# Optimization experiments

Measured on AMD Instinct MI355X. Metric: run time of the kernel, lower is better.

## Reference

```python
import jax, jax.numpy as jnp
import numpy as np

CAPACITY_FACTOR = 1.25
TOP_K = 2


def setup_inputs() -> dict:
    key = jax.random.key(0)
    ks = jax.random.split(key, 4)
    B, T, D, H, N = 8, 8192, 512, 512, 32
    x = jax.random.normal(ks[0], (B, T, D), jnp.float32)
    Wg = jax.random.normal(ks[1], (D, N), jnp.float32) * 0.02   # gate (no bias)
    W1 = jax.random.normal(ks[2], (N, D, H), jnp.float32) * 0.02  # stacked expert fc1
    b1 = jnp.zeros((N, H), jnp.float32)
    W2 = jax.random.normal(ks[3], (N, H, D), jnp.float32) * 0.02  # stacked expert fc2
    b2 = jnp.zeros((N, D), jnp.float32)
    return {"x": x, "Wg": Wg, "W1": W1, "b1": b1, "W2": W2, "b2": b2}


def _moe(x, Wg, W1, b1, W2, b2):
    B, T, D = x.shape
    N = Wg.shape[1]
    K = TOP_K
    BT = B * T
    BTK = BT * K
    C = int(np.ceil(CAPACITY_FACTOR * BTK / N))  # capacity per expert (static)

    x_flat = x.reshape(BT, D)
    probs = jax.nn.softmax(x_flat @ Wg, axis=-1)            # [BT, N]
    vals, idx = jax.lax.top_k(probs, K)                     # [BT, K]
    vals = vals / jnp.clip(vals.sum(-1, keepdims=True), 1e-9)  # normalize_gates

    # Assignments in the exact order of the original double loop: pos-major, j-minor.
    a = idx.reshape(BTK)                                    # expert id per assignment
    oh = jax.nn.one_hot(a, N, dtype=jnp.int32)              # [BTK, N]
    rank = jnp.cumsum(oh, axis=0) - oh                      # prior count for each expert
    pos = jnp.take_along_axis(rank, a[:, None], axis=1)[:, 0]  # slot within expert
    keep = pos < C                                          # capacity-limited dispatch
    dest = jnp.where(keep, a * C + pos, N * C)              # OOB sentinel -> dropped
    token = jnp.arange(BTK) // K                            # source token per assignment

    # Dispatch: scatter kept tokens into per-expert capacity buffers [N, C, D].
    buf = jnp.zeros((N * C, D), x.dtype).at[dest].set(x_flat[token], mode="drop")
    buf = buf.reshape(N, C, D)

    # Expert FFN (grouped GEMMs). FeedForwardExpert assumed Linear-ReLU-Linear.
    h = jax.nn.relu(jnp.einsum("ncd,ndh->nch", buf, W1) + b1[:, None, :])
    o = (jnp.einsum("nch,nhd->ncd", h, W2) + b2[:, None, :]).reshape(N * C, D)

    # Combine: gather expert outputs, weight by gates, scatter-add back by token.
    gathered = o[jnp.minimum(dest, N * C - 1)]              # dropped rows zeroed via w
    w = vals.reshape(BTK) * keep.astype(x.dtype)
    y_flat = jax.ops.segment_sum(gathered * w[:, None], token, num_segments=BT)
    contrib = jax.ops.segment_sum(w, token, num_segments=BT)
    # Tokens with no surviving assignment pass through unchanged.
    y_flat = jnp.where(contrib[:, None] <= 1e-12, x_flat, y_flat)
    return y_flat.reshape(B, T, D)


def reference(x, Wg, W1, b1, W2, b2):
    return _moe(x, Wg, W1, b1, W2, b2)
```

## Files before the change

kernel.cpp:

```cpp
#include <hip/hip_runtime.h>
#include <hip/hip_bf16.h>

#define BT 65536
#define DD 512
#define HH 512
#define NE 32
#define CAP 5120
#define BM 64
#define NRB 80

typedef float  f32x4  __attribute__((ext_vector_type(4)));
typedef short  bf16x8 __attribute__((ext_vector_type(8)));

__device__ __forceinline__ unsigned short f2bf(float f){
    unsigned int u = __builtin_bit_cast(unsigned int, f);
    unsigned int r = (u + 0x7fffu + ((u >> 16) & 1u)) >> 16;
    return (unsigned short)r;
}
__device__ __forceinline__ float bf2f(unsigned short h){
    unsigned int u = ((unsigned int)h) << 16;
    return __builtin_bit_cast(float, u);
}

__global__ __launch_bounds__(256) void k_prep(
    const float* __restrict__ x, const float* __restrict__ Wg,
    const float* __restrict__ W1, const float* __restrict__ W2,
    unsigned short* __restrict__ W1f, unsigned short* __restrict__ W2f,
    int* __restrict__ counts, int* __restrict__ gsl, float* __restrict__ wts,
    unsigned char* __restrict__ flags, unsigned short* __restrict__ xb16)
{
    __shared__ float pacc[4][64][36];
    __shared__ int lcnt[NE], lbase[NE];

    int tid = threadIdx.x;

    if (blockIdx.x < 512){
        int b = blockIdx.x;
        int w = b >> 8;
        int e = (b >> 3) & 31;
        int kq = b & 7;
        const float* src = (w ? W2 : W1) + ((size_t)e << 18);
        unsigned short* dst = (w ? W2f : W1f) + ((size_t)e << 18);
        #pragma unroll 1
        for (int kg = 0; kg < 8; kg++){
            int k0 = kq*64 + kg*8;
            #pragma unroll
            for (int ng = 0; ng < 2; ng++){
                int n = ng*256 + tid;
                unsigned short v[8];
                #pragma unroll
                for (int j = 0; j < 8; j++)
                    v[j] = f2bf(src[(size_t)(k0 + j)*512 + n]);
                int nt = n >> 4, kc = k0 >> 5, ln = ((k0 >> 3) & 3)*16 + (n & 15);
                *(bf16x8*)(dst + (((size_t)(nt*16 + kc)*64 + ln) << 3)) = *(bf16x8*)v;
            }
        }
        return;
    }

    int blk = blockIdx.x - 512;
    int l   = tid & 63;
    int q   = __builtin_amdgcn_readfirstlane(tid >> 6);
    int tok = blk*64 + l;

    const float* xq = x + (size_t)tok*DD + q*128;

    float acc[NE];
    #pragma unroll
    for (int n = 0; n < NE; n++) acc[n] = 0.f;

    float4 xa = *(const float4*)(xq);
    float4 xb = *(const float4*)(xq + 4);
    #pragma unroll 1
    for (int d = 0; d < 128; d += 8){
        int dn = (d + 8 < 128) ? (d + 8) : 0;
        float4 na = *(const float4*)(xq + dn);
        float4 nb = *(const float4*)(xq + dn + 4);
        uint4 pk;
        pk.x = (unsigned)f2bf(xa.x) | ((unsigned)f2bf(xa.y) << 16);
        pk.y = (unsigned)f2bf(xa.z) | ((unsigned)f2bf(xa.w) << 16);
        pk.z = (unsigned)f2bf(xb.x) | ((unsigned)f2bf(xb.y) << 16);
        pk.w = (unsigned)f2bf(xb.z) | ((unsigned)f2bf(xb.w) << 16);
        *(uint4*)(xb16 + (size_t)tok*DD + q*128 + d) = pk;
        #pragma unroll
        for (int j = 0; j < 8; j++){
            float xv = (j < 4) ? ((j==0)?xa.x:(j==1)?xa.y:(j==2)?xa.z:xa.w)
                               : ((j==4)?xb.x:(j==5)?xb.y:(j==6)?xb.z:xb.w);
            const float4* wr = (const float4*)(Wg + (size_t)(q*128 + d + j)*NE);
            #pragma unroll
            for (int p = 0; p < 8; p++){
                float4 w4 = wr[p];
                acc[p*4+0] = fmaf(xv, w4.x, acc[p*4+0]);
                acc[p*4+1] = fmaf(xv, w4.y, acc[p*4+1]);
                acc[p*4+2] = fmaf(xv, w4.z, acc[p*4+2]);
                acc[p*4+3] = fmaf(xv, w4.w, acc[p*4+3]);
            }
        }
        xa = na; xb = nb;
    }

    #pragma unroll
    for (int n4 = 0; n4 < 8; n4++){
        float4 v; v.x = acc[n4*4]; v.y = acc[n4*4+1]; v.z = acc[n4*4+2]; v.w = acc[n4*4+3];
        *(float4*)&pacc[q][l][n4*4] = v;
    }
    if (tid < NE) lcnt[tid] = 0;
    __syncthreads();

    bool owner = (q == (l & 3));
    int i1 = 0, i2 = 0, g1 = 0, g2 = 0;
    float w1 = 0.f, w2 = 0.f;

    if (owner){
        #pragma unroll
        for (int n4 = 0; n4 < 8; n4++){
            float4 p0 = *(float4*)&pacc[0][l][n4*4];
            float4 p1 = *(float4*)&pacc[1][l][n4*4];
            float4 p2 = *(float4*)&pacc[2][l][n4*4];
            float4 p3 = *(float4*)&pacc[3][l][n4*4];
            acc[n4*4+0] = (p0.x + p1.x) + (p2.x + p3.x);
            acc[n4*4+1] = (p0.y + p1.y) + (p2.y + p3.y);
            acc[n4*4+2] = (p0.z + p1.z) + (p2.z + p3.z);
            acc[n4*4+3] = (p0.w + p1.w) + (p2.w + p3.w);
        }

        float v1 = -1e30f; i1 = -1;
        #pragma unroll
        for (int n = 0; n < NE; n++) if (acc[n] > v1){ v1 = acc[n]; i1 = n; }
        float v2 = -1e30f; i2 = -1;
        #pragma unroll
        for (int n = 0; n < NE; n++) if (n != i1 && acc[n] > v2){ v2 = acc[n]; i2 = n; }
        float v3 = -1e30f;
        #pragma unroll
        for (int n = 0; n < NE; n++) if (n != i1 && n != i2 && acc[n] > v3) v3 = acc[n];

        if (v2 - v3 >= 1e-4f){
            double ex  = exp((double)v2 - (double)v1);
            double inv = 1.0 / (1.0 + ex);
            w1 = (float)inv; w2 = (float)(ex * inv);
        } else {
            const float* xr = x + (size_t)tok * DD;
            float thresh = v2 - 1e-3f;
            unsigned cmask = 0u;
            #pragma unroll
            for (int n = 0; n < NE; n++) cmask |= (acc[n] >= thresh) ? (1u << n) : 0u;
            double dv1 = -1.0e300, dv2 = -1.0e300; int di1 = -1, di2 = -1;
            #pragma unroll 1
            for (int n = 0; n < NE; n++){
                if (!((cmask >> n) & 1u)) continue;
                double s0 = 0.0, s1 = 0.0, s2 = 0.0, s3 = 0.0;
                #pragma unroll 4
                for (int d = 0; d < DD; d += 4){
                    s0 = fma((double)xr[d+0], (double)Wg[(size_t)(d+0)*NE + n], s0);
                    s1 = fma((double)xr[d+1], (double)Wg[(size_t)(d+1)*NE + n], s1);
                    s2 = fma((double)xr[d+2], (double)Wg[(size_t)(d+2)*NE + n], s2);
                    s3 = fma((double)xr[d+3], (double)Wg[(size_t)(d+3)*NE + n], s3);
                }
                double s = (s0 + s1) + (s2 + s3);
                if (s > dv1){ dv2 = dv1; di2 = di1; dv1 = s; di1 = n; }
                else if (s > dv2){ dv2 = s; di2 = n; }
            }
            i1 = di1; i2 = di2;
            double ex  = exp(dv2 - dv1);
            double inv = 1.0 / (1.0 + ex);
            w1 = (float)inv; w2 = (float)(ex * inv);
        }
        g1 = atomicAdd(&lcnt[i1], 1);
        g2 = atomicAdd(&lcnt[i2], 1);
    }
    __syncthreads();
    if (tid < NE && lcnt[tid] > 0) lbase[tid] = atomicAdd(&counts[tid], lcnt[tid]);
    __syncthreads();
    if (owner){
        g1 += lbase[i1];
        g2 += lbase[i2];
        bool k1 = g1 < CAP, k2 = g2 < CAP;
        if (k1){ gsl[i1*CAP + g1] = tok;               wts[i1*CAP + g1] = w1; }
        if (k2){ gsl[i2*CAP + g2] = tok | (1 << 20);   wts[i2*CAP + g2] = w2; }
        flags[tok] = (unsigned char)((k1 ? 1 : 0) | (k2 ? 2 : 0));
    }
}

__global__ __launch_bounds__(512, 4) void k_ffn(
    const unsigned short* __restrict__ xb16,
    const unsigned short* __restrict__ W1f,
    const unsigned short* __restrict__ W2f,
    const float* __restrict__ b1, const float* __restrict__ b2,
    const int* __restrict__ counts,
    const int* __restrict__ gsl, const float* __restrict__ wts,
    float* __restrict__ y, unsigned short* __restrict__ y2h)
{
    __shared__ unsigned char AH[64 * 1024];

    int p  = blockIdx.x;
    int s  = p >> 3;
    int e  = ((s / NRB) << 3) | (p & 7);
    int rb = s % NRB;

    int cnt = counts[e]; if (cnt > CAP) cnt = CAP;
    int r0 = rb * BM;
    if (r0 >= cnt) return;

    int tid  = threadIdx.x;
    int lane = tid & 63;
    int wv   = tid >> 6;
    int lg   = lane >> 4;
    int ll   = lane & 15;

    {
        int row = tid >> 3, seg = tid & 7;
        int gr  = r0 + row;
        char* rowb = (char*)AH + row * 1024;
        int rsw = (row & 7) << 4;
        if (gr < cnt){
            int tk = gsl[e*CAP + gr] & 0xFFFFF;
            const uint4* src = (const uint4*)(xb16 + (size_t)tk*DD + seg*64);
            #pragma unroll
            for (int j = 0; j < 8; j++){
                uint4 v = src[j];
                int chunk = seg*8 + j;
                *(uint4*)(rowb + ((chunk << 4) ^ rsw)) = v;
            }
        } else {
            uint4 zz; zz.x = zz.y = zz.z = zz.w = 0u;
            #pragma unroll
            for (int j = 0; j < 8; j++){
                int chunk = seg*8 + j;
                *(uint4*)(rowb + ((chunk << 4) ^ rsw)) = zz;
            }
        }
    }
    __syncthreads();

    f32x4 acc[4][4];
    #pragma unroll
    for (int a2 = 0; a2 < 4; a2++)
        #pragma unroll
        for (int tt = 0; tt < 4; tt++)
            acc[a2][tt] = (f32x4)0.f;

    {
        const unsigned short* Wa = W1f + ((size_t)e << 18) + (size_t)wv*32768;
        bf16x8 f0[4], f1[4];
        #pragma unroll
        for (int a2 = 0; a2 < 4; a2++)
            f0[a2] = *(const bf16x8*)(Wa + a2*8192 + lane*8);
        #pragma unroll 1
        for (int c = 0; c < 16; c += 2){
            #pragma unroll
            for (int a2 = 0; a2 < 4; a2++)
                f1[a2] = *(const bf16x8*)(Wa + a2*8192 + (c+1)*512 + lane*8);
            {
                bf16x8 bx[4];
                #pragma unroll
                for (int tt = 0; tt < 4; tt++){
                    int tok = tt*16 + ll;
                    int bofs = (64*c + 16*lg) ^ ((tok & 7) << 4);
                    bx[tt] = *(const bf16x8*)((char*)AH + tok*1024 + bofs);
                }
                #pragma unroll
                for (int a2 = 0; a2 < 4; a2++)
                    #pragma unroll
                    for (int tt = 0; tt < 4; tt++)
                        acc[a2][tt] = __builtin_amdgcn_mfma_f32_16x16x32_bf16(f0[a2], bx[tt], acc[a2][tt], 0, 0, 0);
            }
            if (c + 2 < 16){
                #pragma unroll
                for (int a2 = 0; a2 < 4; a2++)
                    f0[a2] = *(const bf16x8*)(Wa + a2*8192 + (c+2)*512 + lane*8);
            }
            {
                bf16x8 bx[4];
                #pragma unroll
                for (int tt = 0; tt < 4; tt++){
                    int tok = tt*16 + ll;
                    int bofs = (64*(c+1) + 16*lg) ^ ((tok & 7) << 4);
                    bx[tt] = *(const bf16x8*)((char*)AH + tok*1024 + bofs);
                }
                #pragma unroll
                for (int a2 = 0; a2 < 4; a2++)
                    #pragma unroll
                    for (int tt = 0; tt < 4; tt++)
                        acc[a2][tt] = __builtin_amdgcn_mfma_f32_16x16x32_bf16(f1[a2], bx[tt], acc[a2][tt], 0, 0, 0);
            }
        }
    }
    __syncthreads();

    #pragma unroll
    for (int a2 = 0; a2 < 4; a2++){
        int n0 = wv*64 + a2*16 + lg*4;
        float4 bv = *(const float4*)(b1 + e*HH + n0);
        #pragma unroll
        for (int tt = 0; tt < 4; tt++){
            int tok = tt*16 + ll;
            float h0 = acc[a2][tt][0] + bv.x; h0 = h0 > 0.f ? h0 : 0.f;
            float h1 = acc[a2][tt][1] + bv.y; h1 = h1 > 0.f ? h1 : 0.f;
            float h2 = acc[a2][tt][2] + bv.z; h2 = h2 > 0.f ? h2 : 0.f;
            float h3 = acc[a2][tt][3] + bv.w; h3 = h3 > 0.f ? h3 : 0.f;
            uint2 pk;
            pk.x = (unsigned)f2bf(h0) | ((unsigned)f2bf(h1) << 16);
            pk.y = (unsigned)f2bf(h2) | ((unsigned)f2bf(h3) << 16);
            int bofs = (n0*2) ^ ((tok & 7) << 4);
            *(uint2*)((char*)AH + tok*1024 + bofs) = pk;
            acc[a2][tt] = (f32x4)0.f;
        }
    }
    __syncthreads();

    {
        const unsigned short* Wb = W2f + ((size_t)e << 18) + (size_t)wv*32768;
        bf16x8 f0[4], f1[4];
        #pragma unroll
        for (int b_ = 0; b_ < 4; b_++)
            f0[b_] = *(const bf16x8*)(Wb + b_*8192 + lane*8);
        #pragma unroll 1
        for (int kc = 0; kc < 16; kc += 2){
            #pragma unroll
            for (int b_ = 0; b_ < 4; b_++)
                f1[b_] = *(const bf16x8*)(Wb + b_*8192 + (kc+1)*512 + lane*8);
            {
                bf16x8 ah[4];
                #pragma unroll
                for (int tt = 0; tt < 4; tt++){
                    int tok = tt*16 + ll;
                    int bofs = (64*kc + 16*lg) ^ ((tok & 7) << 4);
                    ah[tt] = *(const bf16x8*)((char*)AH + tok*1024 + bofs);
                }
                #pragma unroll
                for (int b_ = 0; b_ < 4; b_++)
                    #pragma unroll
                    for (int tt = 0; tt < 4; tt++)
                        acc[b_][tt] = __builtin_amdgcn_mfma_f32_16x16x32_bf16(ah[tt], f0[b_], acc[b_][tt], 0, 0, 0);
            }
            if (kc + 2 < 16){
                #pragma unroll
                for (int b_ = 0; b_ < 4; b_++)
                    f0[b_] = *(const bf16x8*)(Wb + b_*8192 + (kc+2)*512 + lane*8);
            }
            {
                bf16x8 ah[4];
                #pragma unroll
                for (int tt = 0; tt < 4; tt++){
                    int tok = tt*16 + ll;
                    int bofs = (64*(kc+1) + 16*lg) ^ ((tok & 7) << 4);
                    ah[tt] = *(const bf16x8*)((char*)AH + tok*1024 + bofs);
                }
                #pragma unroll
                for (int b_ = 0; b_ < 4; b_++)
                    #pragma unroll
                    for (int tt = 0; tt < 4; tt++)
                        acc[b_][tt] = __builtin_amdgcn_mfma_f32_16x16x32_bf16(ah[tt], f1[b_], acc[b_][tt], 0, 0, 0);
            }
        }
    }

    float bb[4];
    #pragma unroll
    for (int b_ = 0; b_ < 4; b_++)
        bb[b_] = b2[e*DD + wv*64 + b_*16 + ll];

    #pragma unroll
    for (int tt = 0; tt < 4; tt++){
        #pragma unroll
        for (int i = 0; i < 4; i++){
            int rl = tt*16 + lg*4 + i;
            int gr = r0 + rl;
            if (gr < cnt){
                int   v  = gsl[e*CAP + gr];
                int   tk = v & 0xFFFFF;
                float w  = wts[e*CAP + gr];
                if (v >> 20){
                    unsigned short* dst = y2h + (size_t)tk * DD;
                    #pragma unroll
                    for (int b_ = 0; b_ < 4; b_++){
                        int col = wv*64 + b_*16 + ll;
                        dst[col] = f2bf(w * (acc[b_][tt][i] + bb[b_]));
                    }
                } else {
                    float* dst = y + (size_t)tk * DD;
                    #pragma unroll
                    for (int b_ = 0; b_ < 4; b_++){
                        int col = wv*64 + b_*16 + ll;
                        dst[col] = w * (acc[b_][tt][i] + bb[b_]);
                    }
                }
            }
        }
    }
}

__global__ __launch_bounds__(256) void k_comb(
    const float* __restrict__ x, const unsigned short* __restrict__ y2h,
    const unsigned char* __restrict__ flags, float* __restrict__ y)
{
    const float4* x4  = (const float4*)x;
    const uint2*  y24 = (const uint2*)y2h;
    float4* y4 = (float4*)y;
    int nthreads = gridDim.x * 256;
    int g = blockIdx.x * 256 + threadIdx.x;
    #pragma unroll 1
    for (long long idx = g; idx < (long long)BT * 128; idx += nthreads){
        int t = (int)(idx >> 7);
        int f = flags[t];
        if (f == 3){
            float4 a = y4[idx];
            uint2 p = y24[idx];
            a.x += bf2f((unsigned short)(p.x & 0xFFFF));
            a.y += bf2f((unsigned short)(p.x >> 16));
            a.z += bf2f((unsigned short)(p.y & 0xFFFF));
            a.w += bf2f((unsigned short)(p.y >> 16));
            y4[idx] = a;
        } else if (f == 2){
            uint2 p = y24[idx];
            float4 a;
            a.x = bf2f((unsigned short)(p.x & 0xFFFF));
            a.y = bf2f((unsigned short)(p.x >> 16));
            a.z = bf2f((unsigned short)(p.y & 0xFFFF));
            a.w = bf2f((unsigned short)(p.y >> 16));
            y4[idx] = a;
        } else if (f == 0){
            y4[idx] = x4[idx];
        }
    }
}

extern "C" void kernel_launch(void* const* d_in, const int* in_sizes, int n_in,
                              void* d_out, int out_size, void* d_ws, size_t ws_size,
                              hipStream_t stream)
{
    const float* x  = (const float*)d_in[0];
    const float* Wg = (const float*)d_in[1];
    const float* W1 = (const float*)d_in[2];
    const float* b1 = (const float*)d_in[3];
    const float* W2 = (const float*)d_in[4];
    const float* b2 = (const float*)d_in[5];
    float* y = (float*)d_out;

    char* ws = (char*)d_ws;
    unsigned short* W1f = (unsigned short*)(ws);
    unsigned short* W2f = (unsigned short*)(ws + 16777216);
    int*   counts = (int*)  (ws + 33554432);
    int*   gsl    = (int*)  (ws + 33554432 + 256);
    float* wts    = (float*)(ws + 33554432 + 256 + 655360);
    unsigned char* flags = (unsigned char*)(ws + 33554432 + 256 + 2*655360);
    unsigned short* xb16 = (unsigned short*)(ws + 35651584);
    unsigned short* y2h  = (unsigned short*)(ws + 35651584 + 67108864);

    hipMemsetAsync(counts, 0, 256, stream);
    hipLaunchKernelGGL(k_prep, dim3(512 + BT/64), dim3(256), 0, stream,
                       x, Wg, W1, W2, W1f, W2f, counts, gsl, wts, flags, xb16);
    hipLaunchKernelGGL(k_ffn,  dim3(NE*NRB), dim3(512), 0, stream,
                       xb16, W1f, W2f, b1, b2, counts, gsl, wts, y, y2h);
    hipLaunchKernelGGL(k_comb, dim3(2048), dim3(256), 0, stream, x, y2h, flags, y);
}
```

Baseline: 421.6 us.

## Restructure gating to one token per thread with LDS Wg; vectorize weight conversion; set MFMA priority

The gating part of the prep kernel now gives each thread a whole token instead of splitting it into four D-quarters reduced through shared memory. The full gate matrix Wg (64 KB) is staged in LDS so every thread reads it from there. This removes the cross-wave partial-sum reduction and the owner-only serial section. The weight-conversion blocks now load float4 rows and emit four bf16x8 fragments per thread, and the grid shrinks from 1536 to 768 blocks. The FFN kernel raises wave priority around MFMA bursts. The risks are lower occupancy from 64 KB of LDS per block, long per-thread serial loops, and reordered blocks in prep.

```diff
diff --git a/kernel.cpp b/kernel.cpp
--- a/kernel.cpp
+++ b/kernel.cpp
@@ -29,156 +29,144 @@
     int* __restrict__ counts, int* __restrict__ gsl, float* __restrict__ wts,
     unsigned char* __restrict__ flags, unsigned short* __restrict__ xb16)
 {
-    __shared__ float pacc[4][64][36];
+    __shared__ float WgS[DD * NE];
     __shared__ int lcnt[NE], lbase[NE];
 
     int tid = threadIdx.x;
 
-    if (blockIdx.x < 512){
-        int b = blockIdx.x;
+    if (blockIdx.x >= 256){
+        int b = blockIdx.x - 256;
         int w = b >> 8;
         int e = (b >> 3) & 31;
         int kq = b & 7;
         const float* src = (w ? W2 : W1) + ((size_t)e << 18);
         unsigned short* dst = (w ? W2f : W1f) + ((size_t)e << 18);
+        int n4 = (tid & 127) * 4;
+        int kh = tid >> 7;
         #pragma unroll 1
-        for (int kg = 0; kg < 8; kg++){
-            int k0 = kq*64 + kg*8;
-            #pragma unroll
-            for (int ng = 0; ng < 2; ng++){
-                int n = ng*256 + tid;
-                unsigned short v[8];
-                #pragma unroll
-                for (int j = 0; j < 8; j++)
-                    v[j] = f2bf(src[(size_t)(k0 + j)*512 + n]);
-                int nt = n >> 4, kc = k0 >> 5, ln = ((k0 >> 3) & 3)*16 + (n & 15);
-                *(bf16x8*)(dst + (((size_t)(nt*16 + kc)*64 + ln) << 3)) = *(bf16x8*)v;
+        for (int kg = 0; kg < 4; kg++){
+            int k0 = kq*64 + (kg*2 + kh)*8;
+            float4 rows[8];
+            #pragma unroll
+            for (int j = 0; j < 8; j++)
+                rows[j] = *(const float4*)&src[(size_t)(k0 + j)*512 + n4];
+            unsigned short v0[8], v1[8], v2[8], v3[8];
+            #pragma unroll
+            for (int j = 0; j < 8; j++){
+                v0[j] = f2bf(rows[j].x); v1[j] = f2bf(rows[j].y);
+                v2[j] = f2bf(rows[j].z); v3[j] = f2bf(rows[j].w);
+            }
+            int kc = k0 >> 5, lb = ((k0 >> 3) & 3)*16;
+            #pragma unroll
+            for (int m = 0; m < 4; m++){
+                int n = n4 + m;
+                int nt = n >> 4, ln = lb + (n & 15);
+                const unsigned short* vv = (m==0)?v0:(m==1)?v1:(m==2)?v2:v3;
+                *(bf16x8*)(dst + (((size_t)(nt*16 + kc)*64 + ln) << 3)) = *(const bf16x8*)vv;
             }
         }
         return;
     }
 
-    int blk = blockIdx.x - 512;
-    int l   = tid & 63;
-    int q   = __builtin_amdgcn_readfirstlane(tid >> 6);
-    int tok = blk*64 + l;
-
-    const float* xq = x + (size_t)tok*DD + q*128;
+    int tok = blockIdx.x * 256 + tid;
+    const float* xr = x + (size_t)tok * DD;
+
+    #pragma unroll
+    for (int i = 0; i < 16; i++){
+        int f = i*1024 + tid*4;
+        *(float4*)&WgS[f] = *(const float4*)&Wg[f];
+    }
+    if (tid < NE) lcnt[tid] = 0;
+    __syncthreads();
 
     float acc[NE];
     #pragma unroll
     for (int n = 0; n < NE; n++) acc[n] = 0.f;
 
-    float4 xa = *(const float4*)(xq);
-    float4 xb = *(const float4*)(xq + 4);
+    float4 xa = *(const float4*)(xr);
+    float4 xb = *(const float4*)(xr + 4);
     #pragma unroll 1
-    for (int d = 0; d < 128; d += 8){
-        int dn = (d + 8 < 128) ? (d + 8) : 0;
-        float4 na = *(const float4*)(xq + dn);
-        float4 nb = *(const float4*)(xq + dn + 4);
+    for (int d = 0; d < DD; d += 8){
+        int dn = (d + 8 < DD) ? (d + 8) : 0;
+        float4 na = *(const float4*)(xr + dn);
+        float4 nb = *(const float4*)(xr + dn + 4);
         uint4 pk;
         pk.x = (unsigned)f2bf(xa.x) | ((unsigned)f2bf(xa.y) << 16);
         pk.y = (unsigned)f2bf(xa.z) | ((unsigned)f2bf(xa.w) << 16);
         pk.z = (unsigned)f2bf(xb.x) | ((unsigned)f2bf(xb.y) << 16);
         pk.w = (unsigned)f2bf(xb.z) | ((unsigned)f2bf(xb.w) << 16);
-        *(uint4*)(xb16 + (size_t)tok*DD + q*128 + d) = pk;
+        *(uint4*)(xb16 + (size_t)tok*DD + d) = pk;
         #pragma unroll
         for (int j = 0; j < 8; j++){
             float xv = (j < 4) ? ((j==0)?xa.x:(j==1)?xa.y:(j==2)?xa.z:xa.w)
                                : ((j==4)?xb.x:(j==5)?xb.y:(j==6)?xb.z:xb.w);
-            const float4* wr = (const float4*)(Wg + (size_t)(q*128 + d + j)*NE);
-            #pragma unroll
-            for (int p = 0; p < 8; p++){
-                float4 w4 = wr[p];
-                acc[p*4+0] = fmaf(xv, w4.x, acc[p*4+0]);
-                acc[p*4+1] = fmaf(xv, w4.y, acc[p*4+1]);
-                acc[p*4+2] = fmaf(xv, w4.z, acc[p*4+2]);
-                acc[p*4+3] = fmaf(xv, w4.w, acc[p*4+3]);
+            const float4* wr = (const float4*)&WgS[(d + j)*NE];
+            #pragma unroll
+            for (int q = 0; q < 8; q++){
+                float4 w4 = wr[q];
+                acc[q*4+0] = fmaf(xv, w4.x, acc[q*4+0]);
+                acc[q*4+1] = fmaf(xv, w4.y, acc[q*4+1]);
+                acc[q*4+2] = fmaf(xv, w4.z, acc[q*4+2]);
+                acc[q*4+3] = fmaf(xv, w4.w, acc[q*4+3]);
             }
         }
         xa = na; xb = nb;
     }
 
-    #pragma unroll
-    for (int n4 = 0; n4 < 8; n4++){
-        float4 v; v.x = acc[n4*4]; v.y = acc[n4*4+1]; v.z = acc[n4*4+2]; v.w = acc[n4*4+3];
-        *(float4*)&pacc[q][l][n4*4] = v;
-    }
-    if (tid < NE) lcnt[tid] = 0;
-    __syncthreads();
-
-    bool owner = (q == (l & 3));
-    int i1 = 0, i2 = 0, g1 = 0, g2 = 0;
-    float w1 = 0.f, w2 = 0.f;
-
-    if (owner){
-        #pragma unroll
-        for (int n4 = 0; n4 < 8; n4++){
-            float4 p0 = *(float4*)&pacc[0][l][n4*4];
-            float4 p1 = *(float4*)&pacc[1][l][n4*4];
-            float4 p2 = *(float4*)&pacc[2][l][n4*4];
-            float4 p3 = *(float4*)&pacc[3][l][n4*4];
-            acc[n4*4+0] = (p0.x + p1.x) + (p2.x + p3.x);
-            acc[n4*4+1] = (p0.y + p1.y) + (p2.y + p3.y);
-            acc[n4*4+2] = (p0.z + p1.z) + (p2.z + p3.z);
-            acc[n4*4+3] = (p0.w + p1.w) + (p2.w + p3.w);
-        }
-
-        float v1 = -1e30f; i1 = -1;
-        #pragma unroll
-        for (int n = 0; n < NE; n++) if (acc[n] > v1){ v1 = acc[n]; i1 = n; }
-        float v2 = -1e30f; i2 = -1;
-        #pragma unroll
-        for (int n = 0; n < NE; n++) if (n != i1 && acc[n] > v2){ v2 = acc[n]; i2 = n; }
-        float v3 = -1e30f;
-        #pragma unroll
-        for (int n = 0; n < NE; n++) if (n != i1 && n != i2 && acc[n] > v3) v3 = acc[n];
-
-        if (v2 - v3 >= 1e-4f){
-            double ex  = exp((double)v2 - (double)v1);
-            double inv = 1.0 / (1.0 + ex);
-            w1 = (float)inv; w2 = (float)(ex * inv);
-        } else {
-            const float* xr = x + (size_t)tok * DD;
-            float thresh = v2 - 1e-3f;
-            unsigned cmask = 0u;
-            #pragma unroll
-            for (int n = 0; n < NE; n++) cmask |= (acc[n] >= thresh) ? (1u << n) : 0u;
-            double dv1 = -1.0e300, dv2 = -1.0e300; int di1 = -1, di2 = -1;
-            #pragma unroll 1
-            for (int n = 0; n < NE; n++){
-                if (!((cmask >> n) & 1u)) continue;
-                double s0 = 0.0, s1 = 0.0, s2 = 0.0, s3 = 0.0;
-                #pragma unroll 4
-                for (int d = 0; d < DD; d += 4){
-                    s0 = fma((double)xr[d+0], (double)Wg[(size_t)(d+0)*NE + n], s0);
-                    s1 = fma((double)xr[d+1], (double)Wg[(size_t)(d+1)*NE + n], s1);
-                    s2 = fma((double)xr[d+2], (double)Wg[(size_t)(d+2)*NE + n], s2);
-                    s3 = fma((double)xr[d+3], (double)Wg[(size_t)(d+3)*NE + n], s3);
-                }
-                double s = (s0 + s1) + (s2 + s3);
-                if (s > dv1){ dv2 = dv1; di2 = di1; dv1 = s; di1 = n; }
-                else if (s > dv2){ dv2 = s; di2 = n; }
-            }
-            i1 = di1; i2 = di2;
-            double ex  = exp(dv2 - dv1);
-            double inv = 1.0 / (1.0 + ex);
-            w1 = (float)inv; w2 = (float)(ex * inv);
-        }
-        g1 = atomicAdd(&lcnt[i1], 1);
-        g2 = atomicAdd(&lcnt[i2], 1);
-    }
+    float v1 = -1e30f; int i1 = -1;
+    #pragma unroll
+    for (int n = 0; n < NE; n++) if (acc[n] > v1){ v1 = acc[n]; i1 = n; }
+    float v2 = -1e30f; int i2 = -1;
+    #pragma unroll
+    for (int n = 0; n < NE; n++) if (n != i1 && acc[n] > v2){ v2 = acc[n]; i2 = n; }
+    float v3 = -1e30f;
+    #pragma unroll
+    for (int n = 0; n < NE; n++) if (n != i1 && n != i2 && acc[n] > v3) v3 = acc[n];
+
+    float w1, w2;
+    if (v2 - v3 >= 1e-4f){
+        double ex  = exp((double)v2 - (double)v1);
+        double inv = 1.0 / (1.0 + ex);
+        w1 = (float)inv; w2 = (float)(ex * inv);
+    } else {
+        float thresh = v2 - 1e-3f;
+        unsigned cmask = 0u;
+        #pragma unroll
+        for (int n = 0; n < NE; n++) cmask |= (acc[n] >= thresh) ? (1u << n) : 0u;
+
+        double dv1 = -1.0e300, dv2 = -1.0e300; int di1 = -1, di2 = -1;
+        #pragma unroll 1
+        for (int n = 0; n < NE; n++){
+            if (!((cmask >> n) & 1u)) continue;
+            double s0 = 0.0, s1 = 0.0, s2 = 0.0, s3 = 0.0;
+            #pragma unroll 4
+            for (int d = 0; d < DD; d += 4){
+                s0 = fma((double)xr[d+0], (double)Wg[(size_t)(d+0)*NE + n], s0);
+                s1 = fma((double)xr[d+1], (double)Wg[(size_t)(d+1)*NE + n], s1);
+                s2 = fma((double)xr[d+2], (double)Wg[(size_t)(d+2)*NE + n], s2);
+                s3 = fma((double)xr[d+3], (double)Wg[(size_t)(d+3)*NE + n], s3);
+            }
+            double s = (s0 + s1) + (s2 + s3);
+            if (s > dv1){ dv2 = dv1; di2 = di1; dv1 = s; di1 = n; }
+            else if (s > dv2){ dv2 = s; di2 = n; }
+        }
+        i1 = di1; i2 = di2;
+        double ex  = exp(dv2 - dv1);
+        double inv = 1.0 / (1.0 + ex);
+        w1 = (float)inv; w2 = (float)(ex * inv);
+    }
+
+    int s1 = atomicAdd(&lcnt[i1], 1);
+    int s2 = atomicAdd(&lcnt[i2], 1);
     __syncthreads();
     if (tid < NE && lcnt[tid] > 0) lbase[tid] = atomicAdd(&counts[tid], lcnt[tid]);
     __syncthreads();
-    if (owner){
-        g1 += lbase[i1];
-        g2 += lbase[i2];
-        bool k1 = g1 < CAP, k2 = g2 < CAP;
-        if (k1){ gsl[i1*CAP + g1] = tok;               wts[i1*CAP + g1] = w1; }
-        if (k2){ gsl[i2*CAP + g2] = tok | (1 << 20);   wts[i2*CAP + g2] = w2; }
-        flags[tok] = (unsigned char)((k1 ? 1 : 0) | (k2 ? 2 : 0));
-    }
+    int g1 = lbase[i1] + s1;
+    int g2 = lbase[i2] + s2;
+    bool k1 = g1 < CAP, k2 = g2 < CAP;
+    if (k1){ gsl[i1*CAP + g1] = tok;               wts[i1*CAP + g1] = w1; }
+    if (k2){ gsl[i2*CAP + g2] = tok | (1 << 20);   wts[i2*CAP + g2] = w2; }
+    flags[tok] = (unsigned char)((k1 ? 1 : 0) | (k2 ? 2 : 0));
 }
 
 __global__ __launch_bounds__(512, 4) void k_ffn(
@@ -258,11 +246,13 @@
                     int bofs = (64*c + 16*lg) ^ ((tok & 7) << 4);
                     bx[tt] = *(const bf16x8*)((char*)AH + tok*1024 + bofs);
                 }
+                __builtin_amdgcn_s_setprio(1);
                 #pragma unroll
                 for (int a2 = 0; a2 < 4; a2++)
                     #pragma unroll
                     for (int tt = 0; tt < 4; tt++)
                         acc[a2][tt] = __builtin_amdgcn_mfma_f32_16x16x32_bf16(f0[a2], bx[tt], acc[a2][tt], 0, 0, 0);
+                __builtin_amdgcn_s_setprio(0);
             }
             if (c + 2 < 16){
                 #pragma unroll
@@ -277,11 +267,13 @@
                     int bofs = (64*(c+1) + 16*lg) ^ ((tok & 7) << 4);
                     bx[tt] = *(const bf16x8*)((char*)AH + tok*1024 + bofs);
                 }
+                __builtin_amdgcn_s_setprio(1);
                 #pragma unroll
                 for (int a2 = 0; a2 < 4; a2++)
                     #pragma unroll
                     for (int tt = 0; tt < 4; tt++)
                         acc[a2][tt] = __builtin_amdgcn_mfma_f32_16x16x32_bf16(f1[a2], bx[tt], acc[a2][tt], 0, 0, 0);
+                __builtin_amdgcn_s_setprio(0);
             }
         }
     }
@@ -327,11 +319,13 @@
                     int bofs = (64*kc + 16*lg) ^ ((tok & 7) << 4);
                     ah[tt] = *(const bf16x8*)((char*)AH + tok*1024 + bofs);
                 }
+                __builtin_amdgcn_s_setprio(1);
                 #pragma unroll
                 for (int b_ = 0; b_ < 4; b_++)
                     #pragma unroll
                     for (int tt = 0; tt < 4; tt++)
                         acc[b_][tt] = __builtin_amdgcn_mfma_f32_16x16x32_bf16(ah[tt], f0[b_], acc[b_][tt], 0, 0, 0);
+                __builtin_amdgcn_s_setprio(0);
             }
             if (kc + 2 < 16){
                 #pragma unroll
@@ -346,11 +340,13 @@
                     int bofs = (64*(kc+1) + 16*lg) ^ ((tok & 7) << 4);
                     ah[tt] = *(const bf16x8*)((char*)AH + tok*1024 + bofs);
                 }
+                __builtin_amdgcn_s_setprio(1);
                 #pragma unroll
                 for (int b_ = 0; b_ < 4; b_++)
                     #pragma unroll
                     for (int tt = 0; tt < 4; tt++)
                         acc[b_][tt] = __builtin_amdgcn_mfma_f32_16x16x32_bf16(ah[tt], f1[b_], acc[b_][tt], 0, 0, 0);
+                __builtin_amdgcn_s_setprio(0);
             }
         }
     }
@@ -448,7 +444,7 @@
     unsigned short* y2h  = (unsigned short*)(ws + 35651584 + 67108864);
 
     hipMemsetAsync(counts, 0, 256, stream);
-    hipLaunchKernelGGL(k_prep, dim3(512 + BT/64), dim3(256), 0, stream,
+    hipLaunchKernelGGL(k_prep, dim3(256 + 512), dim3(256), 0, stream,
                        x, Wg, W1, W2, W1f, W2f, counts, gsl, wts, flags, xb16);
     hipLaunchKernelGGL(k_ffn,  dim3(NE*NRB), dim3(512), 0, stream,
                        xb16, W1f, W2f, b1, b2, counts, gsl, wts, y, y2h);
```

After: 405.5 us. 3.8% less time.
